# Performance work log

Hardware: AMD Instinct MI355X
Metric: run time of the kernel (lower is better)

Reference implementation:

```python
import jax, jax.numpy as jnp
import numpy as np

B, N, D, FH, FW, C = 4, 6, 41, 16, 44, 64
OGH, OGW = 256, 704           # final_dim; downsample=16 -> FH=16, FW=44
NX, NY, NZ = 200, 200, 1      # BEV grid from x/y/zbound
DX = jnp.array([0.5, 0.5, 20.0], dtype=jnp.float32)
BX = jnp.array([-49.75, -49.75, 0.0], dtype=jnp.float32)  # bound lo + dx/2


def make_frustum():
    # (D, FH, FW, 3) of (u_pixel, v_pixel, depth)
    ds = jnp.broadcast_to(jnp.linspace(2.0, 42.0, D)[:, None, None], (D, FH, FW))
    xs = jnp.broadcast_to(jnp.linspace(0.0, OGW - 1.0, FW)[None, None, :], (D, FH, FW))
    ys = jnp.broadcast_to(jnp.linspace(0.0, OGH - 1.0, FH)[None, :, None], (D, FH, FW))
    return jnp.stack([xs, ys, ds], axis=-1).astype(jnp.float32)


def setup_inputs() -> dict:
    key = jax.random.key(0)
    kx, kt = jax.random.split(key)
    x = jax.random.normal(kx, (B, N, D, FH, FW, C), dtype=jnp.float32)
    # camera->ego base rotation: cam z (forward) -> ego x, cam x (right) -> -ego y, cam y (down) -> -ego z
    base = np.array([[0.0, 0.0, 1.0], [-1.0, 0.0, 0.0], [0.0, -1.0, 0.0]], dtype=np.float32)
    rots = np.zeros((B, N, 3, 3), dtype=np.float32)
    for n in range(N):
        th = 2.0 * np.pi * n / N
        c, s = np.cos(th), np.sin(th)
        rz = np.array([[c, -s, 0.0], [s, c, 0.0], [0.0, 0.0, 1.0]], dtype=np.float32)
        rots[:, n] = rz @ base
    trans = 0.5 * jax.random.normal(kt, (B, N, 3), dtype=jnp.float32)
    intr = np.zeros((B, N, 3, 3), dtype=np.float32)
    intr[:, :, 0, 0] = 500.0
    intr[:, :, 1, 1] = 500.0
    intr[:, :, 0, 2] = OGW / 2.0
    intr[:, :, 1, 2] = OGH / 2.0
    intr[:, :, 2, 2] = 1.0
    post_rots = np.broadcast_to(np.eye(3, dtype=np.float32), (B, N, 3, 3)).copy()
    post_trans = np.zeros((B, N, 3), dtype=np.float32)
    return {"x": x, "rots": jnp.asarray(rots), "trans": trans,
            "intrins": jnp.asarray(intr), "post_rots": jnp.asarray(post_rots),
            "post_trans": jnp.asarray(post_trans)}


def get_geometry(rots, trans, intrins, post_rots, post_trans):
    frustum = make_frustum()                                   # (D,FH,FW,3)
    pts = frustum[None, None] - post_trans[:, :, None, None, None, :]
    pts = jnp.einsum('bnij,bndhwj->bndhwi', jnp.linalg.inv(post_rots), pts)
    # undo perspective: (u*d, v*d, d)
    pts = jnp.concatenate([pts[..., :2] * pts[..., 2:3], pts[..., 2:3]], axis=-1)
    combine = rots @ jnp.linalg.inv(intrins)                   # (B,N,3,3)
    pts = jnp.einsum('bnij,bndhwj->bndhwi', combine, pts)
    return pts + trans[:, :, None, None, None, :]              # (B,N,D,FH,FW,3)


def voxel_pooling(geom, x):
    Nprime = B * N * D * FH * FW
    feats = x.reshape(Nprime, C)
    # quantize to voxel indices (torch .long() truncates toward zero)
    g = ((geom - (BX - DX / 2.0)) / DX).astype(jnp.int32).reshape(Nprime, 3)
    batch_ix = jnp.repeat(jnp.arange(B, dtype=jnp.int32), Nprime // B)
    kept = ((g[:, 0] >= 0) & (g[:, 0] < NX) & (g[:, 1] >= 0) & (g[:, 1] < NY)
            & (g[:, 2] >= 0) & (g[:, 2] < NZ))
    # flat index over (B, NZ, NY, NX); invalid points contribute zeros to voxel 0
    idx = ((batch_ix * NZ + g[:, 2]) * NY + g[:, 1]) * NX + g[:, 0]
    idx = jnp.where(kept, idx, 0)
    feats = jnp.where(kept[:, None], feats, 0.0)
    grid = jnp.zeros((B * NZ * NY * NX, C), dtype=feats.dtype).at[idx].add(feats)
    grid = grid.reshape(B, NZ, NY, NX, C).transpose(0, 1, 4, 2, 3)  # (B,NZ,C,NY,NX)
    return grid.reshape(B, NZ * C, NY, NX)  # == torch.cat(unbind(dim=2), 1)


def reference(x, rots, trans, intrins, post_rots, post_trans):
    geom = get_geometry(rots, trans, intrins, post_rots, post_trans)
    return voxel_pooling(geom, x)
```

## Files before the change

kernel.cpp:

```cpp
#include <hip/hip_runtime.h>
#include <hip/hip_bf16.h>

namespace {
constexpr int B = 4, N = 6, D = 41, FH = 16, FW = 44, C = 64;
constexpr int NX = 200, NY = 200;
constexpr int NGROUPS = B * N * D * FW;
constexpr long long ACC_ELEMS = (long long)B * NY * NX * C;
constexpr int PARAMS_PER_CAM = 24;
constexpr int FLAG_IDX = B * N * PARAMS_PER_CAM;
}

__device__ __forceinline__ float ldin(const void* p, size_t idx, int fp32m) {
  return fp32m ? ((const float*)p)[idx]
               : __bfloat162float(((const __hip_bfloat16*)p)[idx]);
}

__device__ __forceinline__ float dot3(float m0, float m1, float m2, float a0,
                                      float a1, float a2) {
  return __fadd_rn(__fadd_rn(__fmul_rn(m0, a0), __fmul_rn(m1, a1)),
                   __fmul_rn(m2, a2));
}

__device__ inline void inv3x3_f64(const float a_[9], float o[9]) {
  double a[9];
  for (int k = 0; k < 9; ++k) a[k] = (double)a_[k];
  double c00 = a[4] * a[8] - a[5] * a[7];
  double c01 = a[5] * a[6] - a[3] * a[8];
  double c02 = a[3] * a[7] - a[4] * a[6];
  double det = a[0] * c00 + a[1] * c01 + a[2] * c02;
  double id = 1.0 / det;
  o[0] = (float)(c00 * id);
  o[1] = (float)((a[2] * a[7] - a[1] * a[8]) * id);
  o[2] = (float)((a[1] * a[5] - a[2] * a[4]) * id);
  o[3] = (float)(c01 * id);
  o[4] = (float)((a[0] * a[8] - a[2] * a[6]) * id);
  o[5] = (float)((a[2] * a[3] - a[0] * a[5]) * id);
  o[6] = (float)(c02 * id);
  o[7] = (float)((a[1] * a[6] - a[0] * a[7]) * id);
  o[8] = (float)((a[0] * a[4] - a[1] * a[3]) * id);
}

__global__ void setup_kernel(const void* rots, const void* trans,
                             const void* intr, const void* prots,
                             const void* ptrans, float* params) {
  int i = threadIdx.x;
  float probe = ((const float*)intr)[0];
  int fp32m = (probe > 100.f && probe < 2000.f) ? 1 : 0;
  if (i == 0) ((int*)params)[FLAG_IDX] = fp32m;
  if (i >= B * N) return;
  float R[9], K[9], PR[9];
  for (int k = 0; k < 9; ++k) {
    R[k] = ldin(rots, (size_t)i * 9 + k, fp32m);
    K[k] = ldin(intr, (size_t)i * 9 + k, fp32m);
    PR[k] = ldin(prots, (size_t)i * 9 + k, fp32m);
  }
  float iPR[9];
  inv3x3_f64(PR, iPR);
  float i00 = __fdiv_rn(1.f, K[0]);
  float i11 = __fdiv_rn(1.f, K[4]);
  float i22 = __fdiv_rn(1.f, K[8]);
  float i01 = __fmul_rn(-i11, __fmul_rn(i00, K[1]));
  float x1 = __fmul_rn(i00, K[2]);
  x1 = __fadd_rn(x1, __fmul_rn(K[5], i01));
  float x2 = __fmul_rn(i11, K[5]);
  float i02 = __fmul_rn(-i22, x1);
  float i12 = __fmul_rn(-i22, x2);
  float iK[9] = {i00, i01, i02, 0.f, i11, i12, 0.f, 0.f, i22};
  float* o = params + i * PARAMS_PER_CAM;
  for (int k = 0; k < 9; ++k) o[k] = iPR[k];
  for (int k = 0; k < 3; ++k) o[9 + k] = ldin(ptrans, (size_t)i * 3 + k, fp32m);
  for (int r = 0; r < 3; ++r)
    for (int c2 = 0; c2 < 3; ++c2)
      o[12 + r * 3 + c2] = dot3(R[r * 3], R[r * 3 + 1], R[r * 3 + 2],
                                iK[c2], iK[3 + c2], iK[6 + c2]);
  for (int k = 0; k < 3; ++k) o[21 + k] = ldin(trans, (size_t)i * 3 + k, fp32m);
}

__global__ void zero_kernel(float4* __restrict__ acc, int n4) {
  int i = blockIdx.x * blockDim.x + threadIdx.x;
  if (i < n4) acc[i] = make_float4(0.f, 0.f, 0.f, 0.f);
}

__global__ __launch_bounds__(256) void scatter_kernel(
    const void* __restrict__ x, const float* __restrict__ params,
    float* __restrict__ acc) {
  int tid = threadIdx.x;
  int c = tid & 63;
  int g = blockIdx.x * 4 + (tid >> 6);
  int w = g % FW;
  int t = g / FW;
  int d = t % D;
  t /= D;
  int n = t % N;
  int b = t / N;
  const float* pr = params + (b * N + n) * PARAMS_PER_CAM;
  int fp32m = ((const int*)params)[FLAG_IDX];
  float u = (w == FW - 1) ? 703.0f : (float)((double)w * (703.0 / 43.0));
  float dep = (float)(2 + d);
  float ax = __fsub_rn(u, pr[9]);
  float az = __fsub_rn(dep, pr[11]);
  const size_t hstride = (size_t)FW * C;
  const size_t base = ((((size_t)(b * N + n) * D + d) * FH) * FW + w) * C + c;
  float sum = 0.f;
  int curvox = -1;
  for (int h = 0; h < FH; ++h) {
    float v = (float)(17 * h);
    float ay = __fsub_rn(v, pr[10]);
    float qx = dot3(pr[0], pr[1], pr[2], ax, ay, az);
    float qy = dot3(pr[3], pr[4], pr[5], ax, ay, az);
    float qz = dot3(pr[6], pr[7], pr[8], ax, ay, az);
    qx = __fmul_rn(qx, qz);
    qy = __fmul_rn(qy, qz);
    float gx = __fadd_rn(dot3(pr[12], pr[13], pr[14], qx, qy, qz), pr[21]);
    float gy = __fadd_rn(dot3(pr[15], pr[16], pr[17], qx, qy, qz), pr[22]);
    float gz = __fadd_rn(dot3(pr[18], pr[19], pr[20], qx, qy, qz), pr[23]);
    int ix = (int)__fdiv_rn(__fsub_rn(gx, -50.0f), 0.5f);
    int iy = (int)__fdiv_rn(__fsub_rn(gy, -50.0f), 0.5f);
    int iz = (int)__fdiv_rn(__fsub_rn(gz, -10.0f), 20.0f);
    if (ix >= 0 && ix < NX && iy >= 0 && iy < NY && iz == 0) {
      int vox = (b * NY + iy) * NX + ix;
      if (vox != curvox) {
        if (curvox >= 0)
          atomicAdd(acc + (size_t)curvox * C + c, sum);
        sum = 0.f;
        curvox = vox;
      }
      sum = __fadd_rn(sum, ldin(x, base + (size_t)h * hstride, fp32m));
    }
  }
  if (curvox >= 0) atomicAdd(acc + (size_t)curvox * C + c, sum);
}

__global__ __launch_bounds__(256) void finalize_kernel(
    const float* __restrict__ acc, void* __restrict__ out,
    const float* __restrict__ params) {
  int fp32m = ((const int*)params)[FLAG_IDX];
  int y = blockIdx.x % NY;
  int b = blockIdx.x / NY;
  __shared__ float tile[NX * 65];
  const float4* src = (const float4*)(acc + (size_t)(b * NY + y) * NX * C);
  for (int i = threadIdx.x; i < NX * 16; i += 256) {
    float4 vv = src[i];
    int xx = i >> 4, c4 = i & 15;
    float* dst = &tile[xx * 65 + c4 * 4];
    dst[0] = vv.x;
    dst[1] = vv.y;
    dst[2] = vv.z;
    dst[3] = vv.w;
  }
  __syncthreads();
  for (int i = threadIdx.x; i < C * (NX / 4); i += 256) {
    int cc = i / (NX / 4), k = i % (NX / 4);
    int xx = 4 * k;
    float4 vv;
    vv.x = tile[xx * 65 + cc];
    vv.y = tile[(xx + 1) * 65 + cc];
    vv.z = tile[(xx + 2) * 65 + cc];
    vv.w = tile[(xx + 3) * 65 + cc];
    size_t o = ((size_t)(b * C + cc) * NY + y) * NX + xx;
    if (fp32m) {
      *(float4*)((float*)out + o) = vv;
    } else {
      __hip_bfloat16* op = (__hip_bfloat16*)out + o;
      op[0] = __float2bfloat16(vv.x);
      op[1] = __float2bfloat16(vv.y);
      op[2] = __float2bfloat16(vv.z);
      op[3] = __float2bfloat16(vv.w);
    }
  }
}

extern "C" void kernel_launch(void* const* d_in, const int* in_sizes, int n_in,
                              void* d_out, int out_size, void* d_ws,
                              size_t ws_size, hipStream_t stream) {
  const void* x = d_in[0];
  const void* rots = d_in[1];
  const void* trans = d_in[2];
  const void* intr = d_in[3];
  const void* prots = d_in[4];
  const void* ptrans = d_in[5];

  float* acc = (float*)d_ws;
  float* params = acc + ACC_ELEMS;

  setup_kernel<<<1, 64, 0, stream>>>(rots, trans, intr, prots, ptrans, params);

  int n4 = (int)(ACC_ELEMS / 4);
  zero_kernel<<<(n4 + 255) / 256, 256, 0, stream>>>((float4*)acc, n4);

  scatter_kernel<<<NGROUPS / 4, 256, 0, stream>>>(x, params, acc);

  finalize_kernel<<<B * NY, 256, 0, stream>>>(acc, d_out, params);
}
```

Before: 319.7 us.

## Split scatter into geometry compaction pass and segment-list gather kernel

```diff
diff --git a/kernel.cpp b/kernel.cpp
--- a/kernel.cpp
+++ b/kernel.cpp
@@ -8,6 +8,8 @@
 constexpr long long ACC_ELEMS = (long long)B * NY * NX * C;
 constexpr int PARAMS_PER_CAM = 24;
 constexpr int FLAG_IDX = B * N * PARAMS_PER_CAM;
+constexpr int CTR_OFF = 640;
+constexpr int SEG_OFF = 704;
 }
 
 __device__ __forceinline__ float ldin(const void* p, size_t idx, int fp32m) {
@@ -19,6 +21,26 @@
                                       float a1, float a2) {
   return __fadd_rn(__fadd_rn(__fmul_rn(m0, a0), __fmul_rn(m1, a1)),
                    __fmul_rn(m2, a2));
+}
+
+__device__ __forceinline__ int voxel_of(const float* pr, float ax, float az,
+                                        int b, int h) {
+  float v = (float)(17 * h);
+  float ay = __fsub_rn(v, pr[10]);
+  float qx = dot3(pr[0], pr[1], pr[2], ax, ay, az);
+  float qy = dot3(pr[3], pr[4], pr[5], ax, ay, az);
+  float qz = dot3(pr[6], pr[7], pr[8], ax, ay, az);
+  qx = __fmul_rn(qx, qz);
+  qy = __fmul_rn(qy, qz);
+  float gx = __fadd_rn(dot3(pr[12], pr[13], pr[14], qx, qy, qz), pr[21]);
+  float gy = __fadd_rn(dot3(pr[15], pr[16], pr[17], qx, qy, qz), pr[22]);
+  float gz = __fadd_rn(dot3(pr[18], pr[19], pr[20], qx, qy, qz), pr[23]);
+  int ix = (int)__fdiv_rn(__fsub_rn(gx, -50.0f), 0.5f);
+  int iy = (int)__fdiv_rn(__fsub_rn(gy, -50.0f), 0.5f);
+  int iz = (int)__fdiv_rn(__fsub_rn(gz, -10.0f), 20.0f);
+  if (ix >= 0 && ix < NX && iy >= 0 && iy < NY && iz == 0)
+    return (b * NY + iy) * NX + ix;
+  return -1;
 }
 
 __device__ inline void inv3x3_f64(const float a_[9], float o[9]) {
@@ -46,7 +68,10 @@
   int i = threadIdx.x;
   float probe = ((const float*)intr)[0];
   int fp32m = (probe > 100.f && probe < 2000.f) ? 1 : 0;
-  if (i == 0) ((int*)params)[FLAG_IDX] = fp32m;
+  if (i == 0) {
+    ((int*)params)[FLAG_IDX] = fp32m;
+    ((int*)params)[CTR_OFF] = 0;
+  }
   if (i >= B * N) return;
   float R[9], K[9], PR[9];
   for (int k = 0; k < 9; ++k) {
@@ -71,8 +96,8 @@
   for (int k = 0; k < 3; ++k) o[9 + k] = ldin(ptrans, (size_t)i * 3 + k, fp32m);
   for (int r = 0; r < 3; ++r)
     for (int c2 = 0; c2 < 3; ++c2)
-      o[12 + r * 3 + c2] = dot3(R[r * 3], R[r * 3 + 1], R[r * 3 + 2],
-                                iK[c2], iK[3 + c2], iK[6 + c2]);
+      o[12 + r * 3 + c2] = dot3(R[r * 3], R[r * 3 + 1], R[r * 3 + 2], iK[c2],
+                                iK[3 + c2], iK[6 + c2]);
   for (int k = 0; k < 3; ++k) o[21 + k] = ldin(trans, (size_t)i * 3 + k, fp32m);
 }
 
@@ -81,54 +106,93 @@
   if (i < n4) acc[i] = make_float4(0.f, 0.f, 0.f, 0.f);
 }
 
-__global__ __launch_bounds__(256) void scatter_kernel(
+__global__ __launch_bounds__(256) void geom_kernel(float* params) {
+  int g = blockIdx.x * blockDim.x + threadIdx.x;
+  int lane = threadIdx.x & 63;
+  int* counter = (int*)params + CTR_OFF;
+  int2* segs = (int2*)((int*)params + SEG_OFF);
+  int nseg = 0;
+  const float* pr = nullptr;
+  float ax = 0.f, az = 0.f;
+  int b = 0;
+  if (g < NGROUPS) {
+    int w = g % FW;
+    int t = g / FW;
+    int d = t % D;
+    t /= D;
+    int n = t % N;
+    b = t / N;
+    pr = params + (b * N + n) * PARAMS_PER_CAM;
+    float u = (w == FW - 1) ? 703.0f : (float)((double)w * (703.0 / 43.0));
+    float dep = (float)(2 + d);
+    ax = __fsub_rn(u, pr[9]);
+    az = __fsub_rn(dep, pr[11]);
+    int curvox = -1;
+    for (int h = 0; h < FH; ++h) {
+      int vox = voxel_of(pr, ax, az, b, h);
+      if (vox >= 0 && vox != curvox) {
+        ++nseg;
+        curvox = vox;
+      }
+    }
+  }
+  int incl = nseg;
+#pragma unroll
+  for (int s = 1; s < 64; s <<= 1) {
+    int y = __shfl_up(incl, s, 64);
+    if (lane >= s) incl += y;
+  }
+  int total = __shfl(incl, 63, 64);
+  int excl = incl - nseg;
+  int basev = 0;
+  if (lane == 63 && total > 0) basev = atomicAdd(counter, total);
+  basev = __shfl(basev, 63, 64);
+  if (g < NGROUPS && nseg > 0) {
+    int curvox = -1, mask = 0, k = 0;
+    for (int h = 0; h < FH; ++h) {
+      int vox = voxel_of(pr, ax, az, b, h);
+      if (vox >= 0) {
+        if (vox != curvox) {
+          if (curvox >= 0) {
+            segs[basev + excl + k] = make_int2((g << 16) | mask, curvox);
+            ++k;
+          }
+          curvox = vox;
+          mask = 0;
+        }
+        mask |= (1 << h);
+      }
+    }
+    if (curvox >= 0) segs[basev + excl + k] = make_int2((g << 16) | mask, curvox);
+  }
+}
+
+__global__ __launch_bounds__(256) void gather_kernel(
     const void* __restrict__ x, const float* __restrict__ params,
     float* __restrict__ acc) {
-  int tid = threadIdx.x;
-  int c = tid & 63;
-  int g = blockIdx.x * 4 + (tid >> 6);
-  int w = g % FW;
-  int t = g / FW;
-  int d = t % D;
-  t /= D;
-  int n = t % N;
-  int b = t / N;
-  const float* pr = params + (b * N + n) * PARAMS_PER_CAM;
+  int lane = threadIdx.x & 63;
+  int wid = blockIdx.x * (blockDim.x >> 6) + (threadIdx.x >> 6);
+  int nwaves = gridDim.x * (blockDim.x >> 6);
+  int total = ((const int*)params)[CTR_OFF];
   int fp32m = ((const int*)params)[FLAG_IDX];
-  float u = (w == FW - 1) ? 703.0f : (float)((double)w * (703.0 / 43.0));
-  float dep = (float)(2 + d);
-  float ax = __fsub_rn(u, pr[9]);
-  float az = __fsub_rn(dep, pr[11]);
-  const size_t hstride = (size_t)FW * C;
-  const size_t base = ((((size_t)(b * N + n) * D + d) * FH) * FW + w) * C + c;
-  float sum = 0.f;
-  int curvox = -1;
-  for (int h = 0; h < FH; ++h) {
-    float v = (float)(17 * h);
-    float ay = __fsub_rn(v, pr[10]);
-    float qx = dot3(pr[0], pr[1], pr[2], ax, ay, az);
-    float qy = dot3(pr[3], pr[4], pr[5], ax, ay, az);
-    float qz = dot3(pr[6], pr[7], pr[8], ax, ay, az);
-    qx = __fmul_rn(qx, qz);
-    qy = __fmul_rn(qy, qz);
-    float gx = __fadd_rn(dot3(pr[12], pr[13], pr[14], qx, qy, qz), pr[21]);
-    float gy = __fadd_rn(dot3(pr[15], pr[16], pr[17], qx, qy, qz), pr[22]);
-    float gz = __fadd_rn(dot3(pr[18], pr[19], pr[20], qx, qy, qz), pr[23]);
-    int ix = (int)__fdiv_rn(__fsub_rn(gx, -50.0f), 0.5f);
-    int iy = (int)__fdiv_rn(__fsub_rn(gy, -50.0f), 0.5f);
-    int iz = (int)__fdiv_rn(__fsub_rn(gz, -10.0f), 20.0f);
-    if (ix >= 0 && ix < NX && iy >= 0 && iy < NY && iz == 0) {
-      int vox = (b * NY + iy) * NX + ix;
-      if (vox != curvox) {
-        if (curvox >= 0)
-          atomicAdd(acc + (size_t)curvox * C + c, sum);
-        sum = 0.f;
-        curvox = vox;
-      }
-      sum = __fadd_rn(sum, ldin(x, base + (size_t)h * hstride, fp32m));
-    }
-  }
-  if (curvox >= 0) atomicAdd(acc + (size_t)curvox * C + c, sum);
+  const int2* segs = (const int2*)((const int*)params + SEG_OFF);
+  for (int s = wid; s < total; s += nwaves) {
+    int2 e = segs[s];
+    int g = ((unsigned)e.x) >> 16;
+    int mask = e.x & 0xffff;
+    int vox = e.y;
+    int w = g % FW;
+    int t = g / FW;
+    size_t base = ((size_t)t * FH * FW + w) * (size_t)C + lane;
+    float sum = 0.f;
+    int m = mask;
+    while (m) {
+      int h = __builtin_ctz(m);
+      m &= m - 1;
+      sum = __fadd_rn(sum, ldin(x, base + (size_t)(h * FW * C), fp32m));
+    }
+    atomicAdd(acc + (size_t)vox * C + lane, sum);
+  }
 }
 
 __global__ __launch_bounds__(256) void finalize_kernel(
@@ -188,7 +252,9 @@
   int n4 = (int)(ACC_ELEMS / 4);
   zero_kernel<<<(n4 + 255) / 256, 256, 0, stream>>>((float4*)acc, n4);
 
-  scatter_kernel<<<NGROUPS / 4, 256, 0, stream>>>(x, params, acc);
+  geom_kernel<<<(NGROUPS + 255) / 256, 256, 0, stream>>>(params);
+
+  gather_kernel<<<1024, 256, 0, stream>>>(x, params, acc);
 
   finalize_kernel<<<B * NY, 256, 0, stream>>>(acc, d_out, params);
 }
```

Result: slower. 366.3 us (+14.6%).
